# Kernel optimization log

Hardware: AMD Instinct MI355X
Metric: run time of the kernel (lower is better)

## Reference

```python
import jax, jax.numpy as jnp
import numpy as np

HEAD_NUM = 12
HEAD_SIZE = 64
INPUT_DIM = 768
BATCH = 2
SEQ = 2048
NEG = 1e12


def setup_inputs() -> dict:
    key = jax.random.key(0)
    k1, k2, k3 = jax.random.split(key, 3)
    x = jax.random.normal(k1, (BATCH, SEQ, INPUT_DIM), dtype=jnp.float32)
    W = jax.random.normal(k2, (INPUT_DIM, HEAD_NUM * HEAD_SIZE * 2), dtype=jnp.float32) * 0.02
    b = jax.random.normal(k3, (HEAD_NUM * HEAD_SIZE * 2,), dtype=jnp.float32) * 0.02
    mask = jnp.ones((BATCH, SEQ), dtype=jnp.int32)
    return {"x": x, "W": W, "b": b, "mask": mask}


def _rope_tables(n, d, dtype):
    # SinusoidalPositionEmbedding(head_size, 'zero'): pos[..., 0::2]=sin, 1::2=cos
    pos = jnp.arange(n, dtype=dtype)
    freqs = jnp.power(10000.0, -2.0 * jnp.arange(d // 2, dtype=dtype) / d)
    ang = pos[:, None] * freqs[None, :]  # [n, d/2]
    # K.repeat_elements(pos[..., 1::2], 2, -1) -> each cos value repeated twice
    cos_pos = jnp.repeat(jnp.cos(ang), 2, axis=-1)  # [n, d]
    sin_pos = jnp.repeat(jnp.sin(ang), 2, axis=-1)  # [n, d]
    return cos_pos[None, :, None, :], sin_pos[None, :, None, :]  # [1,n,1,d]


def _rotate_half(t):
    # stack([-t[...,1::2], t[...,::2]], -1).reshape(t.shape)
    t2 = jnp.stack([-t[..., 1::2], t[..., 0::2]], axis=-1)
    return t2.reshape(t.shape)


def reference(x, W, b, mask):
    bsz, n, _ = x.shape
    proj = (x @ W + b).reshape(bsz, n, HEAD_NUM, 2 * HEAD_SIZE)  # [b,n,h,2d]
    qw, kw = proj[..., :HEAD_SIZE], proj[..., HEAD_SIZE:]
    cos_pos, sin_pos = _rope_tables(n, HEAD_SIZE, x.dtype)
    qw = qw * cos_pos + _rotate_half(qw) * sin_pos
    kw = kw * cos_pos + _rotate_half(kw) * sin_pos
    logits = jnp.einsum('bmhd,bnhd->bhmn', qw, kw)  # [b,h,m,n]
    m = mask.astype(logits.dtype)
    logits = logits - (1.0 - m[:, None, :, None]) * NEG  # mask query axis (dim 2)
    logits = logits - (1.0 - m[:, None, None, :]) * NEG  # mask key axis (dim 3)
    tri = jnp.triu(jnp.ones((n, n), dtype=logits.dtype))  # band_part(0,-1): keep m<=n
    logits = logits - (1.0 - tri) * NEG
    return logits / (HEAD_SIZE ** 0.5)
```

## Files before the change

kernel.cpp:

```cpp
#include <hip/hip_runtime.h>

#define SEQ    2048
#define IND    768
#define NPROJ  1536
#define BHN    24
#define NEGV   1000000000000.0f

typedef __attribute__((ext_vector_type(4))) float f32x4;
typedef __attribute__((ext_vector_type(8))) short s16x8;
typedef __attribute__((ext_vector_type(8))) unsigned short u16x8;
typedef __attribute__((ext_vector_type(4))) unsigned short u16x4;

__device__ __forceinline__ unsigned short f2bf(float f) {
  unsigned int u = __builtin_bit_cast(unsigned int, f);
  u += 0x7fffu + ((u >> 16) & 1u);
  return (unsigned short)(u >> 16);
}

__global__ __launch_bounds__(256) void k_prep(const float* __restrict__ x,
                                              const float* __restrict__ W,
                                              unsigned short* __restrict__ xb,
                                              unsigned short* __restrict__ Wt,
                                              float* __restrict__ cosT,
                                              float* __restrict__ sinT) {
  __shared__ float Ws[64][65];
  const int bid = blockIdx.x;
  const int tid = threadIdx.x;

  if (bid < 1536) {
    int i = (bid * 256 + tid) * 8;
    float4 a = *(const float4*)(x + i);
    float4 b = *(const float4*)(x + i + 4);
    u16x8 o;
    o[0] = f2bf(a.x); o[1] = f2bf(a.y); o[2] = f2bf(a.z); o[3] = f2bf(a.w);
    o[4] = f2bf(b.x); o[5] = f2bf(b.y); o[6] = f2bf(b.z); o[7] = f2bf(b.w);
    *(u16x8*)(xb + i) = o;
  } else if (bid < 1824) {
    int tb = bid - 1536;
    int nt = tb % 24, kt = tb / 24;
    int n0 = nt * 64, k0 = kt * 64;
    int cr = tid >> 4;
    int cc = (tid & 15) * 4;
#pragma unroll
    for (int it = 0; it < 4; ++it) {
      int kr = it * 16 + cr;
      float4 v = *(const float4*)(W + (size_t)(k0 + kr) * NPROJ + n0 + cc);
      Ws[kr][cc + 0] = v.x; Ws[kr][cc + 1] = v.y;
      Ws[kr][cc + 2] = v.z; Ws[kr][cc + 3] = v.w;
    }
    __syncthreads();
#pragma unroll
    for (int it = 0; it < 4; ++it) {
      int nl = it * 16 + cr;
      u16x4 o;
#pragma unroll
      for (int q = 0; q < 4; ++q) o[q] = f2bf(Ws[cc + q][nl]);
      *(u16x4*)(Wt + (size_t)(n0 + nl) * IND + k0 + cc) = o;
    }
  } else {
    int i = (bid - 1824) * 256 + tid;
    int s = i >> 5, f = i & 31;
    float freq = exp2f(-(float)f * (13.287712379549449f / 32.0f));
    float ang = (float)s * freq;
    float sv, cv;
    sincosf(ang, &sv, &cv);
    cosT[i] = cv; sinT[i] = sv;
  }
}

__global__ __launch_bounds__(256, 2) void k_proj(const unsigned short* __restrict__ xb,
                                                 const unsigned short* __restrict__ Wt,
                                                 const float* __restrict__ bias,
                                                 unsigned short* __restrict__ Qb,
                                                 unsigned short* __restrict__ Kb,
                                                 const float* __restrict__ cosT,
                                                 const float* __restrict__ sinT) {
  __shared__ int4 As4[1024];
  __shared__ int4 Bs4[1024];
  const int tid = threadIdx.x;
  const int m0 = blockIdx.y * 128, n0 = blockIdx.x * 128;
  const int wid = tid >> 6, lane = tid & 63;
  const int wr = wid >> 1, wc = wid & 1;
  const int lr = lane & 15, kg = lane >> 4;

  f32x4 acc[4][4] = {};

  for (int kt = 0; kt < 12; ++kt) {
#pragma unroll
    for (int it = 0; it < 4; ++it) {
      int id = it * 256 + tid;
      int row = id >> 3, cb = id & 7;
      int sw = cb ^ (row & 7);
      As4[row * 8 + sw] = *(const int4*)(xb + (size_t)(m0 + row) * IND + kt * 64 + cb * 8);
      Bs4[row * 8 + sw] = *(const int4*)(Wt + (size_t)(n0 + row) * IND + kt * 64 + cb * 8);
    }
    __syncthreads();
#pragma unroll
    for (int kk = 0; kk < 2; ++kk) {
      s16x8 af[4], bfr[4];
#pragma unroll
      for (int i = 0; i < 4; ++i) {
        int r = wr * 64 + i * 16 + lr;
        af[i] = *(const s16x8*)&As4[r * 8 + ((kk * 4 + kg) ^ (r & 7))];
      }
#pragma unroll
      for (int j = 0; j < 4; ++j) {
        int r = wc * 64 + j * 16 + lr;
        bfr[j] = *(const s16x8*)&Bs4[r * 8 + ((kk * 4 + kg) ^ (r & 7))];
      }
#pragma unroll
      for (int i = 0; i < 4; ++i)
#pragma unroll
        for (int j = 0; j < 4; ++j)
          acc[i][j] = __builtin_amdgcn_mfma_f32_16x16x32_bf16(af[i], bfr[j], acc[i][j], 0, 0, 0);
    }
    __syncthreads();
  }

#pragma unroll
  for (int i = 0; i < 4; ++i) {
    int rowb = m0 + wr * 64 + i * 16 + kg * 4;
#pragma unroll
    for (int j = 0; j < 4; ++j) {
      int col = n0 + wc * 64 + j * 16 + lr;
      float bcol = bias[col];
      int d = col & 63;
      int h = col >> 7;
      bool isq = (col & 64) == 0;
      unsigned short* dst = isq ? Qb : Kb;
#pragma unroll
      for (int r = 0; r < 4; ++r) {
        int m = rowb + r;
        int s = m & (SEQ - 1), bb = m >> 11;
        float v = acc[i][j][r] + bcol;
        float p = __shfl_xor(v, 1);
        int ti = s * 32 + (d >> 1);
        float cv = cosT[ti], sv = sinT[ti];
        float o = (col & 1) ? (v * cv + p * sv) : (v * cv - p * sv);
        dst[((size_t)(bb * 12 + h) * SEQ + s) * 64 + d] = f2bf(o);
      }
    }
  }
}

__global__ __launch_bounds__(256, 2) void k_attn(const unsigned short* __restrict__ Qb,
                                                 const unsigned short* __restrict__ Kb,
                                                 const int* __restrict__ mask,
                                                 float* __restrict__ out) {
  __shared__ int4 smem[2048];
  int4* Qs4 = smem;
  int4* Ks4 = smem + 1024;

  const int b0 = blockIdx.x;
  const int lin = (b0 & 7) * 768 + (b0 >> 3);
  const int bh = lin >> 8;
  const int rem = lin & 255;
  const int mt = rem >> 4, nt = rem & 15;
  const int b = bh / 12;
  const int tid = threadIdx.x;
  const int m0 = mt * 128, n0 = nt * 128;
  const float scale = 0.125f;

  if (nt < mt) {
#pragma unroll
    for (int it = 0; it < 16; ++it) {
      int id = it * 256 + tid;
      int row = id >> 5, c4 = id & 31;
      int gm = m0 + row;
      float rm = (float)mask[b * SEQ + gm];
      int gn0 = n0 + c4 * 4;
      float4 v;
#pragma unroll
      for (int q = 0; q < 4; ++q) {
        float cm = (float)mask[b * SEQ + gn0 + q];
        ((float*)&v)[q] = -(NEGV * ((1.f - rm) + (1.f - cm) + 1.f)) * scale;
      }
      *(float4*)(out + ((size_t)bh * SEQ + gm) * SEQ + gn0) = v;
    }
    return;
  }

  const int wid = tid >> 6, lane = tid & 63;
  const int wr = wid >> 1, wc = wid & 1;
  const int lr = lane & 15, kg = lane >> 4;

#pragma unroll
  for (int it = 0; it < 4; ++it) {
    int id = it * 256 + tid;
    int row = id >> 3, cb = id & 7;
    int sw = cb ^ (row & 7);
    Qs4[row * 8 + sw] = *(const int4*)(Qb + ((size_t)bh * SEQ + m0 + row) * 64 + cb * 8);
    Ks4[row * 8 + sw] = *(const int4*)(Kb + ((size_t)bh * SEQ + n0 + row) * 64 + cb * 8);
  }
  __syncthreads();

  f32x4 acc[4][4] = {};
#pragma unroll
  for (int kk = 0; kk < 2; ++kk) {
    s16x8 af[4], bfr[4];
#pragma unroll
    for (int i = 0; i < 4; ++i) {
      int r = wr * 64 + i * 16 + lr;
      af[i] = *(const s16x8*)&Qs4[r * 8 + ((kk * 4 + kg) ^ (r & 7))];
    }
#pragma unroll
    for (int j = 0; j < 4; ++j) {
      int r = wc * 64 + j * 16 + lr;
      bfr[j] = *(const s16x8*)&Ks4[r * 8 + ((kk * 4 + kg) ^ (r & 7))];
    }
#pragma unroll
    for (int i = 0; i < 4; ++i)
#pragma unroll
      for (int j = 0; j < 4; ++j)
        acc[i][j] = __builtin_amdgcn_mfma_f32_16x16x32_bf16(af[i], bfr[j], acc[i][j], 0, 0, 0);
  }

  __syncthreads();
  float* Cs = (float*)smem;

#pragma unroll
  for (int c = 0; c < 2; ++c) {
    if (wr == c) {
#pragma unroll
      for (int i = 0; i < 4; ++i)
#pragma unroll
        for (int j = 0; j < 4; ++j) {
          int col = wc * 64 + j * 16 + lr;
          int g = col >> 2;
#pragma unroll
          for (int r = 0; r < 4; ++r) {
            int rl = i * 16 + kg * 4 + r;
            int gs = g ^ (rl & 7);
            Cs[rl * 128 + gs * 4 + (col & 3)] = acc[i][j][r];
          }
        }
    }
    __syncthreads();
#pragma unroll
    for (int it = 0; it < 8; ++it) {
      int id = it * 256 + tid;
      int rl = id >> 5, g = id & 31;
      int gs = g ^ (rl & 7);
      float4 v = *(const float4*)&Cs[rl * 128 + gs * 4];
      int gm = m0 + c * 64 + rl;
      int gn0 = n0 + g * 4;
      float rmv = (float)mask[b * SEQ + gm];
      int4 cm = *(const int4*)&mask[b * SEQ + gn0];
      float4 o;
#pragma unroll
      for (int q = 0; q < 4; ++q) {
        int gn = gn0 + q;
        float cmv = (float)((const int*)&cm)[q];
        float pen = (1.f - rmv) + (1.f - cmv) + ((gn < gm) ? 1.f : 0.f);
        ((float*)&o)[q] = (((const float*)&v)[q] - NEGV * pen) * scale;
      }
      *(float4*)(out + ((size_t)bh * SEQ + gm) * SEQ + gn0) = o;
    }
    __syncthreads();
  }
}

extern "C" void kernel_launch(void* const* d_in, const int* in_sizes, int n_in,
                              void* d_out, int out_size, void* d_ws, size_t ws_size,
                              hipStream_t stream) {
  const float* x    = (const float*)d_in[0];
  const float* W    = (const float*)d_in[1];
  const float* bias = (const float*)d_in[2];
  const int*   mask = (const int*)d_in[3];
  float* out = (float*)d_out;

  char* ws = (char*)d_ws;
  unsigned short* xb = (unsigned short*)(ws);
  unsigned short* Wt = (unsigned short*)(ws + 6291456);
  unsigned short* Qb = (unsigned short*)(ws + 6291456 + 2359296);
  unsigned short* Kb = (unsigned short*)(ws + 6291456 + 2359296 + 6291456);
  float* cosT = (float*)(ws + 6291456 + 2359296 + 6291456 + 6291456);
  float* sinT = (float*)(ws + 6291456 + 2359296 + 6291456 + 6291456 + 262144);

  k_prep<<<2080, 256, 0, stream>>>(x, W, xb, Wt, cosT, sinT);
  k_proj<<<dim3(12, 32), 256, 0, stream>>>(xb, Wt, bias, Qb, Kb, cosT, sinT);
  k_attn<<<6144, 256, 0, stream>>>(Qb, Kb, mask, out);
}
```

Before: 109.2 us.

## Use direct global-to-LDS loads, double-buffer projection GEMM, nontemporal logit stores

Tile staging in both the projection and attention kernels now uses global_load_lds, which writes global data straight into LDS in the same swizzled layout instead of going through registers. The projection GEMM gets double-buffered LDS so the next K-slice loads while the current one feeds the MFMAs. Its blocks are also remapped onto a 1D grid so neighbouring tiles land on the same XCD. The attention kernel writes the large fp32 logits output with nontemporal stores to reduce cache pollution, and its launch bound is raised to allow more resident blocks. The risks are doubled LDS in the GEMM, which may lower occupancy, and reliance on barriers to cover the asynchronous LDS loads.

```diff
diff --git a/kernel.cpp b/kernel.cpp
--- a/kernel.cpp
+++ b/kernel.cpp
@@ -15,6 +15,28 @@
   unsigned int u = __builtin_bit_cast(unsigned int, f);
   u += 0x7fffu + ((u >> 16) & 1u);
   return (unsigned short)(u >> 16);
+}
+
+__device__ __forceinline__ void nt_store4(float* p, f32x4 v) {
+  __builtin_nontemporal_store(v, (f32x4*)p);
+}
+
+#define GLOAD_LDS16(g, l)                                              \
+  __builtin_amdgcn_global_load_lds(                                    \
+      (const __attribute__((address_space(1))) void*)(g),              \
+      (__attribute__((address_space(3))) void*)(l), 16, 0, 0)
+
+__device__ __forceinline__ void stage128x64(const unsigned short* __restrict__ src,
+                                            size_t stride, int4* lds, int tid) {
+  const int w = tid >> 6, l = tid & 63;
+#pragma unroll
+  for (int i = 0; i < 4; ++i) {
+    int gb = w * 256 + i * 64;
+    int G = gb + l;
+    int row = G >> 3, g = G & 7;
+    int cb = g ^ (row & 7);
+    GLOAD_LDS16(src + (size_t)row * stride + cb * 8, lds + gb);
+  }
 }
 
 __global__ __launch_bounds__(256) void k_prep(const float* __restrict__ x,
@@ -75,38 +97,46 @@
                                                  unsigned short* __restrict__ Kb,
                                                  const float* __restrict__ cosT,
                                                  const float* __restrict__ sinT) {
-  __shared__ int4 As4[1024];
-  __shared__ int4 Bs4[1024];
+  __shared__ int4 As4[2][1024];
+  __shared__ int4 Bs4[2][1024];
   const int tid = threadIdx.x;
-  const int m0 = blockIdx.y * 128, n0 = blockIdx.x * 128;
+  const int bidl = blockIdx.x;
+  const int bid = (bidl & 7) * 48 + (bidl >> 3);
+  const int nt = bid % 12, mt = bid / 12;
+  const int m0 = mt * 128, n0 = nt * 128;
   const int wid = tid >> 6, lane = tid & 63;
   const int wr = wid >> 1, wc = wid & 1;
   const int lr = lane & 15, kg = lane >> 4;
 
   f32x4 acc[4][4] = {};
 
+  const unsigned short* Abase = xb + (size_t)m0 * IND;
+  const unsigned short* Bbase = Wt + (size_t)n0 * IND;
+
+  stage128x64(Abase, IND, As4[0], tid);
+  stage128x64(Bbase, IND, Bs4[0], tid);
+  __syncthreads();
+
   for (int kt = 0; kt < 12; ++kt) {
-#pragma unroll
-    for (int it = 0; it < 4; ++it) {
-      int id = it * 256 + tid;
-      int row = id >> 3, cb = id & 7;
-      int sw = cb ^ (row & 7);
-      As4[row * 8 + sw] = *(const int4*)(xb + (size_t)(m0 + row) * IND + kt * 64 + cb * 8);
-      Bs4[row * 8 + sw] = *(const int4*)(Wt + (size_t)(n0 + row) * IND + kt * 64 + cb * 8);
-    }
-    __syncthreads();
+    int cur = kt & 1;
+    if (kt < 11) {
+      stage128x64(Abase + (kt + 1) * 64, IND, As4[cur ^ 1], tid);
+      stage128x64(Bbase + (kt + 1) * 64, IND, Bs4[cur ^ 1], tid);
+    }
+    const int4* Ac = As4[cur];
+    const int4* Bc = Bs4[cur];
 #pragma unroll
     for (int kk = 0; kk < 2; ++kk) {
       s16x8 af[4], bfr[4];
 #pragma unroll
       for (int i = 0; i < 4; ++i) {
         int r = wr * 64 + i * 16 + lr;
-        af[i] = *(const s16x8*)&As4[r * 8 + ((kk * 4 + kg) ^ (r & 7))];
+        af[i] = *(const s16x8*)&Ac[r * 8 + ((kk * 4 + kg) ^ (r & 7))];
       }
 #pragma unroll
       for (int j = 0; j < 4; ++j) {
         int r = wc * 64 + j * 16 + lr;
-        bfr[j] = *(const s16x8*)&Bs4[r * 8 + ((kk * 4 + kg) ^ (r & 7))];
+        bfr[j] = *(const s16x8*)&Bc[r * 8 + ((kk * 4 + kg) ^ (r & 7))];
       }
 #pragma unroll
       for (int i = 0; i < 4; ++i)
@@ -143,7 +173,7 @@
   }
 }
 
-__global__ __launch_bounds__(256, 2) void k_attn(const unsigned short* __restrict__ Qb,
+__global__ __launch_bounds__(256, 4) void k_attn(const unsigned short* __restrict__ Qb,
                                                  const unsigned short* __restrict__ Kb,
                                                  const int* __restrict__ mask,
                                                  float* __restrict__ out) {
@@ -169,13 +199,13 @@
       int gm = m0 + row;
       float rm = (float)mask[b * SEQ + gm];
       int gn0 = n0 + c4 * 4;
-      float4 v;
+      f32x4 v;
 #pragma unroll
       for (int q = 0; q < 4; ++q) {
         float cm = (float)mask[b * SEQ + gn0 + q];
-        ((float*)&v)[q] = -(NEGV * ((1.f - rm) + (1.f - cm) + 1.f)) * scale;
-      }
-      *(float4*)(out + ((size_t)bh * SEQ + gm) * SEQ + gn0) = v;
+        v[q] = -(NEGV * ((1.f - rm) + (1.f - cm) + 1.f)) * scale;
+      }
+      nt_store4(out + ((size_t)bh * SEQ + gm) * SEQ + gn0, v);
     }
     return;
   }
@@ -184,14 +214,8 @@
   const int wr = wid >> 1, wc = wid & 1;
   const int lr = lane & 15, kg = lane >> 4;
 
-#pragma unroll
-  for (int it = 0; it < 4; ++it) {
-    int id = it * 256 + tid;
-    int row = id >> 3, cb = id & 7;
-    int sw = cb ^ (row & 7);
-    Qs4[row * 8 + sw] = *(const int4*)(Qb + ((size_t)bh * SEQ + m0 + row) * 64 + cb * 8);
-    Ks4[row * 8 + sw] = *(const int4*)(Kb + ((size_t)bh * SEQ + n0 + row) * 64 + cb * 8);
-  }
+  stage128x64(Qb + ((size_t)bh * SEQ + m0) * 64, 64, Qs4, tid);
+  stage128x64(Kb + ((size_t)bh * SEQ + n0) * 64, 64, Ks4, tid);
   __syncthreads();
 
   f32x4 acc[4][4] = {};
@@ -241,20 +265,20 @@
       int id = it * 256 + tid;
       int rl = id >> 5, g = id & 31;
       int gs = g ^ (rl & 7);
-      float4 v = *(const float4*)&Cs[rl * 128 + gs * 4];
+      f32x4 v = *(const f32x4*)&Cs[rl * 128 + gs * 4];
       int gm = m0 + c * 64 + rl;
       int gn0 = n0 + g * 4;
       float rmv = (float)mask[b * SEQ + gm];
       int4 cm = *(const int4*)&mask[b * SEQ + gn0];
-      float4 o;
+      f32x4 o;
 #pragma unroll
       for (int q = 0; q < 4; ++q) {
         int gn = gn0 + q;
         float cmv = (float)((const int*)&cm)[q];
         float pen = (1.f - rmv) + (1.f - cmv) + ((gn < gm) ? 1.f : 0.f);
-        ((float*)&o)[q] = (((const float*)&v)[q] - NEGV * pen) * scale;
-      }
-      *(float4*)(out + ((size_t)bh * SEQ + gm) * SEQ + gn0) = o;
+        o[q] = (v[q] - NEGV * pen) * scale;
+      }
+      nt_store4(out + ((size_t)bh * SEQ + gm) * SEQ + gn0, o);
     }
     __syncthreads();
   }
@@ -278,6 +302,6 @@
   float* sinT = (float*)(ws + 6291456 + 2359296 + 6291456 + 6291456 + 262144);
 
   k_prep<<<2080, 256, 0, stream>>>(x, W, xb, Wt, cosT, sinT);
-  k_proj<<<dim3(12, 32), 256, 0, stream>>>(xb, Wt, bias, Qb, Kb, cosT, sinT);
+  k_proj<<<384, 256, 0, stream>>>(xb, Wt, bias, Qb, Kb, cosT, sinT);
   k_attn<<<6144, 256, 0, stream>>>(Qb, Kb, mask, out);
 }
```

Result: faster. 103.1 us (-5.5%).
